# Kernel tuning notes

Hardware: AMD Instinct MI355X
Metric: run time of the kernel (lower is better)

The kernel has to match this reference:

```python
import jax, jax.numpy as jnp
import numpy as np

N, DIM = 65536, 512

def setup_inputs() -> dict:
    key = jax.random.key(0)
    k1, k2, k3 = jax.random.split(key, 3)
    x = jax.random.normal(k1, (N, DIM), dtype=jnp.float32)
    x_fit = jax.random.normal(k2, (N, DIM), dtype=jnp.float32)
    # Module registers S_inv = eye(dim); add a small symmetric PSD perturbation
    # so the matrix is non-trivial while staying well-conditioned.
    A = jax.random.normal(k3, (DIM, DIM), dtype=jnp.float32) / jnp.float32(DIM)
    S_inv = jnp.eye(DIM, dtype=jnp.float32) + A @ A.T
    return {"x": x, "x_fit": x_fit, "S_inv": S_inv}

def reference(x, x_fit, S_inv):
    # Squared Mahalanobis distance per row:
    # diag(delta @ S_inv @ delta.T) == sum((delta @ S_inv) * delta, axis=-1)
    delta = x - x_fit                      # [N, d]
    return jnp.einsum('nd,de,ne->n', delta, S_inv, delta)  # [N]
```

## Files before the change

### kernel.cpp

```cpp
#include <hip/hip_runtime.h>
#include <stdint.h>

#define DIM 512
#define ROWS_PER_BLOCK 64
#define N_CHUNKS 32
#define CHUNK_BYTES 8192
#define WS_BYTES (N_CHUNKS * CHUNK_BYTES)
#define N_BUF 4
#define PREFETCH 3

typedef __attribute__((ext_vector_type(4))) float f32x4;
typedef __attribute__((ext_vector_type(2))) float f32x2;
typedef __attribute__((ext_vector_type(4))) int   i32x4;

static __device__ __forceinline__ int kperm(int kk, int q) {
  int g = q >> 3, j = q & 7;
  int r = (j < 4) ? (g * 4 + j) : (16 + g * 4 + (j - 4));
  return kk * 32 + r;
}

__global__ void prep_R(const float* __restrict__ S, uint32_t* __restrict__ ws) {
  int idx = blockIdx.x * blockDim.x + threadIdx.x;
  if (idx >= WS_BYTES / 4) return;
  int b     = idx * 4;
  int chunk = b >> 13;
  int e_l   = (b >> 9) & 15;
  int inrow = b & 511;
  int slot  = inrow >> 4;
  int bia   = inrow & 15;
  int la    = (slot - e_l) & 31;
  int P = la >> 2, g = la & 3;
  int e = chunk * 16 + e_l;
  float v[4];
#pragma unroll
  for (int t = 0; t < 4; ++t) {
    int bb = bia + t;
    int j  = bb & 7;
    int kk = 2 * P + (bb >> 3);
    int k  = kperm(kk, g * 8 + j);
    v[t] = 64.0f * (S[k * DIM + e] - (k == e ? 1.0f : 0.0f));
  }
  int w = __builtin_amdgcn_cvt_pk_fp8_f32(v[0], v[1], 0, false);
  w     = __builtin_amdgcn_cvt_pk_fp8_f32(v[2], v[3], w, true);
  ws[idx] = (uint32_t)w;
}

static __device__ __forceinline__ void stage_chunk(const uint32_t* __restrict__ ws,
                                                   int eb, char* dst, int tid) {
  const uint32_t* src = ws + (size_t)eb * (CHUNK_BYTES / 4);
#pragma unroll
  for (int r = 0; r < 2; ++r) {
    int idx = r * 256 + tid;
    __builtin_amdgcn_global_load_lds(
        (const __attribute__((address_space(1))) void*)(src + idx * 4),
        (__attribute__((address_space(3))) void*)(dst + idx * 16),
        16, 0, 0);
  }
}

template <int KK>
struct P0 {
  static __device__ __forceinline__ void run(const float* __restrict__ xr,
                                             const float* __restrict__ fr,
                                             int g, long long (&fragL)[16], float& sumsq) {
    const float4 a0 = *(const float4*)(xr + KK * 32 + 4 * g);
    const float4 b0 = *(const float4*)(fr + KK * 32 + 4 * g);
    const float4 a1 = *(const float4*)(xr + KK * 32 + 16 + 4 * g);
    const float4 b1 = *(const float4*)(fr + KK * 32 + 16 + 4 * g);
    float d0 = a0.x - b0.x, d1 = a0.y - b0.y, d2 = a0.z - b0.z, d3 = a0.w - b0.w;
    float d4 = a1.x - b1.x, d5 = a1.y - b1.y, d6 = a1.z - b1.z, d7 = a1.w - b1.w;
    sumsq += d0*d0 + d1*d1 + d2*d2 + d3*d3 + d4*d4 + d5*d5 + d6*d6 + d7*d7;
    int lo = __builtin_amdgcn_cvt_pk_fp8_f32(d0, d1, 0, false);
    lo     = __builtin_amdgcn_cvt_pk_fp8_f32(d2, d3, lo, true);
    int hi = __builtin_amdgcn_cvt_pk_fp8_f32(d4, d5, 0, false);
    hi     = __builtin_amdgcn_cvt_pk_fp8_f32(d6, d7, hi, true);
    fragL[KK] = (long long)(((unsigned long long)(unsigned)hi << 32) | (unsigned)lo);
    P0<KK + 1>::run(xr, fr, g, fragL, sumsq);
  }
};
template <>
struct P0<16> {
  static __device__ __forceinline__ void run(const float*, const float*, int,
                                             long long (&)[16], float&) {}
};

template <int P>
struct KLoop {
  static __device__ __forceinline__ void run(const char* __restrict__ rowbase,
                                             int g, int m,
                                             const long long (&fragL)[16],
                                             f32x4& c0, f32x4& c1) {
    int off = ((4 * P + g + m) & 31) * 16;
    i32x4 a = *(const i32x4*)(rowbase + off);
    long long A0 = (long long)(((unsigned long long)(unsigned)a[1] << 32) | (unsigned)a[0]);
    long long A1 = (long long)(((unsigned long long)(unsigned)a[3] << 32) | (unsigned)a[2]);
    c0 = __builtin_amdgcn_mfma_f32_16x16x32_fp8_fp8(A0, fragL[2 * P],     c0, 0, 0, 0);
    c1 = __builtin_amdgcn_mfma_f32_16x16x32_fp8_fp8(A1, fragL[2 * P + 1], c1, 0, 0, 0);
    KLoop<P + 1>::run(rowbase, g, m, fragL, c0, c1);
  }
};
template <>
struct KLoop<8> {
  static __device__ __forceinline__ void run(const char*, int, int,
                                             const long long (&)[16], f32x4&, f32x4&) {}
};

template <int EB>
struct ChunkLoop {
  static __device__ __forceinline__ void run(const uint32_t* __restrict__ ws,
                                             char* __restrict__ sbase,
                                             int tid, int m, int g,
                                             const long long (&fragL)[16], float& part) {
    if constexpr (EB <= N_CHUNKS - 3)
      asm volatile("s_waitcnt vmcnt(4) lgkmcnt(0)" ::: "memory");
    else if constexpr (EB == N_CHUNKS - 2)
      asm volatile("s_waitcnt vmcnt(2) lgkmcnt(0)" ::: "memory");
    else
      asm volatile("s_waitcnt vmcnt(0) lgkmcnt(0)" ::: "memory");
    __builtin_amdgcn_s_barrier();

    if constexpr (EB + PREFETCH < N_CHUNKS)
      stage_chunk(ws, EB + PREFETCH,
                  sbase + ((EB + PREFETCH) & (N_BUF - 1)) * CHUNK_BYTES, tid);

    const char* rowbase = sbase + (EB & (N_BUF - 1)) * CHUNK_BYTES + m * 512;
    f32x4 c0 = {0.f, 0.f, 0.f, 0.f}, c1 = {0.f, 0.f, 0.f, 0.f};
    KLoop<0>::run(rowbase, g, m, fragL, c0, c1);

    constexpr int kk = EB >> 1;
    int src = (int)(fragL[kk] >> ((EB & 1) * 32));
    f32x2 f01 = __builtin_amdgcn_cvt_pk_f32_fp8(src, false);
    f32x2 f23 = __builtin_amdgcn_cvt_pk_f32_fp8(src, true);
    part += (c0[0] + c1[0]) * f01[0] + (c0[1] + c1[1]) * f01[1]
          + (c0[2] + c1[2]) * f23[0] + (c0[3] + c1[3]) * f23[1];

    ChunkLoop<EB + 1>::run(ws, sbase, tid, m, g, fragL, part);
  }
};
template <>
struct ChunkLoop<N_CHUNKS> {
  static __device__ __forceinline__ void run(const uint32_t*, char*, int, int, int,
                                             const long long (&)[16], float&) {}
};

__global__ __launch_bounds__(256, 2)
void mahal_main(const float* __restrict__ X, const float* __restrict__ XF,
                const uint32_t* __restrict__ ws, float* __restrict__ out) {
  __shared__ __align__(16) char sA[N_BUF][CHUNK_BYTES];

  const int tid  = threadIdx.x;
  const int lane = tid & 63;
  const int wv   = tid >> 6;
  const int m    = lane & 15;
  const int g    = lane >> 4;
  const int row  = blockIdx.x * ROWS_PER_BLOCK + wv * 16 + m;

  const float* xr = X  + (size_t)row * DIM;
  const float* fr = XF + (size_t)row * DIM;

  stage_chunk(ws, 0, sA[0], tid);
  stage_chunk(ws, 1, sA[1], tid);
  stage_chunk(ws, 2, sA[2], tid);

  long long fragL[16];
  float sumsq = 0.f;
  P0<0>::run(xr, fr, g, fragL, sumsq);
  sumsq += __shfl_xor(sumsq, 16);
  sumsq += __shfl_xor(sumsq, 32);

  float part = 0.f;
  ChunkLoop<0>::run(ws, &sA[0][0], tid, m, g, fragL, part);

  part += __shfl_xor(part, 16);
  part += __shfl_xor(part, 32);
  if (g == 0) out[row] = sumsq + part * 0.015625f;
}

__global__ void mahal_naive(const float* __restrict__ X, const float* __restrict__ XF,
                            const float* __restrict__ S, float* __restrict__ out, int n) {
  int row = blockIdx.x * blockDim.x + threadIdx.x;
  if (row >= n) return;
  const float* xr = X + (size_t)row * DIM;
  const float* fr = XF + (size_t)row * DIM;
  float acc = 0.f;
  for (int d = 0; d < DIM; ++d) {
    float dd = xr[d] - fr[d];
    float inner = 0.f;
    for (int e = 0; e < DIM; ++e) inner += S[d * DIM + e] * (xr[e] - fr[e]);
    acc += dd * inner;
  }
  out[row] = acc;
}

extern "C" void kernel_launch(void* const* d_in, const int* in_sizes, int n_in,
                              void* d_out, int out_size, void* d_ws, size_t ws_size,
                              hipStream_t stream) {
  const float* X  = (const float*)d_in[0];
  const float* XF = (const float*)d_in[1];
  const float* S  = (const float*)d_in[2];
  float* out = (float*)d_out;
  const int N = in_sizes[0] / DIM;

  if (ws_size < (size_t)WS_BYTES || (N % ROWS_PER_BLOCK) != 0) {
    mahal_naive<<<(N + 63) / 64, 64, 0, stream>>>(X, XF, S, out, N);
    return;
  }

  uint32_t* ws = (uint32_t*)d_ws;
  prep_R<<<(WS_BYTES / 4 + 255) / 256, 256, 0, stream>>>(S, ws);
  mahal_main<<<N / ROWS_PER_BLOCK, 256, 0, stream>>>(X, XF, ws, out);
}
```

Measured before the change: 304.7 us.

## Split delta computation into coalesced fp8 packing kernel before MFMA pass

Adds a pre-pass kernel that reads x and x_fit with fully coalesced vector loads, computes the delta and its squared norm, and writes a packed fp8 fragment image plus per-row sums into workspace. The main MFMA kernel then loads its fragments from this compact image instead of doing strided fp32 loads and conversions. This removes poorly coalesced fp32 traffic from the latency-sensitive main kernel, at the cost of an extra launch and an extra round trip of the fp8 image through memory. The path is only taken when the workspace is large enough.

Measured after the change: 310.6 us. About the same (+1.9%).

```diff
diff --git a/kernel.cpp b/kernel.cpp
--- a/kernel.cpp
+++ b/kernel.cpp
@@ -43,6 +43,41 @@
   int w = __builtin_amdgcn_cvt_pk_fp8_f32(v[0], v[1], 0, false);
   w     = __builtin_amdgcn_cvt_pk_fp8_f32(v[2], v[3], w, true);
   ws[idx] = (uint32_t)w;
+}
+
+__global__ __launch_bounds__(256)
+void delta_pack(const float* __restrict__ X, const float* __restrict__ XF,
+                unsigned long long* __restrict__ img, float* __restrict__ sums,
+                int nrows) {
+  const int lane = threadIdx.x & 63;
+  const int wid  = blockIdx.x * (blockDim.x >> 6) + (threadIdx.x >> 6);
+  const int nw   = gridDim.x * (blockDim.x >> 6);
+  const int g    = lane & 3;
+  const int h    = (lane >> 2) & 1;
+  const int kA   = lane >> 3;
+  for (int row = wid; row < nrows; row += nw) {
+    const f32x4* xq = (const f32x4*)(X  + (size_t)row * DIM);
+    const f32x4* fq = (const f32x4*)(XF + (size_t)row * DIM);
+    f32x4 xa = xq[lane], fa = fq[lane];
+    f32x4 xb = xq[lane + 64], fb = fq[lane + 64];
+    f32x4 dA = xa - fa, dB = xb - fb;
+    float ps = dA[0]*dA[0] + dA[1]*dA[1] + dA[2]*dA[2] + dA[3]*dA[3]
+             + dB[0]*dB[0] + dB[1]*dB[1] + dB[2]*dB[2] + dB[3]*dB[3];
+    int wA = __builtin_amdgcn_cvt_pk_fp8_f32(dA[0], dA[1], 0, false);
+    wA     = __builtin_amdgcn_cvt_pk_fp8_f32(dA[2], dA[3], wA, true);
+    int wB = __builtin_amdgcn_cvt_pk_fp8_f32(dB[0], dB[1], 0, false);
+    wB     = __builtin_amdgcn_cvt_pk_fp8_f32(dB[2], dB[3], wB, true);
+    int pA = __shfl_xor(wA, 4);
+    int pB = __shfl_xor(wB, 4);
+    unsigned long long L;
+    int kk;
+    if (h == 0) { L = ((unsigned long long)(unsigned)pA << 32) | (unsigned)wA; kk = kA; }
+    else        { L = ((unsigned long long)(unsigned)wB << 32) | (unsigned)pB; kk = 8 + kA; }
+    img[(size_t)row * 64 + g * 16 + kk] = L;
+    ps += __shfl_xor(ps, 1);  ps += __shfl_xor(ps, 2);  ps += __shfl_xor(ps, 4);
+    ps += __shfl_xor(ps, 8);  ps += __shfl_xor(ps, 16); ps += __shfl_xor(ps, 32);
+    if (lane == 0) sums[row] = ps;
+  }
 }
 
 static __device__ __forceinline__ void stage_chunk(const uint32_t* __restrict__ ws,
@@ -143,9 +178,12 @@
                                              const long long (&)[16], float&) {}
 };
 
+template <bool FROM_IMG>
 __global__ __launch_bounds__(256, 2)
 void mahal_main(const float* __restrict__ X, const float* __restrict__ XF,
-                const uint32_t* __restrict__ ws, float* __restrict__ out) {
+                const uint32_t* __restrict__ ws,
+                const unsigned long long* __restrict__ img,
+                const float* __restrict__ sums, float* __restrict__ out) {
   __shared__ __align__(16) char sA[N_BUF][CHUNK_BYTES];
 
   const int tid  = threadIdx.x;
@@ -155,25 +193,39 @@
   const int g    = lane >> 4;
   const int row  = blockIdx.x * ROWS_PER_BLOCK + wv * 16 + m;
 
-  const float* xr = X  + (size_t)row * DIM;
-  const float* fr = XF + (size_t)row * DIM;
-
   stage_chunk(ws, 0, sA[0], tid);
   stage_chunk(ws, 1, sA[1], tid);
   stage_chunk(ws, 2, sA[2], tid);
 
   long long fragL[16];
   float sumsq = 0.f;
-  P0<0>::run(xr, fr, g, fragL, sumsq);
-  sumsq += __shfl_xor(sumsq, 16);
-  sumsq += __shfl_xor(sumsq, 32);
+  if constexpr (FROM_IMG) {
+    const i32x4* ib = (const i32x4*)(img + (size_t)row * 64 + (size_t)g * 16);
+    i32x4 t[8];
+#pragma unroll
+    for (int j = 0; j < 8; ++j) t[j] = ib[j];
+#pragma unroll
+    for (int j = 0; j < 8; ++j) {
+      fragL[2 * j]     = (long long)(((unsigned long long)(unsigned)t[j][1] << 32) | (unsigned)t[j][0]);
+      fragL[2 * j + 1] = (long long)(((unsigned long long)(unsigned)t[j][3] << 32) | (unsigned)t[j][2]);
+    }
+  } else {
+    const float* xr = X  + (size_t)row * DIM;
+    const float* fr = XF + (size_t)row * DIM;
+    P0<0>::run(xr, fr, g, fragL, sumsq);
+    sumsq += __shfl_xor(sumsq, 16);
+    sumsq += __shfl_xor(sumsq, 32);
+  }
 
   float part = 0.f;
   ChunkLoop<0>::run(ws, &sA[0][0], tid, m, g, fragL, part);
 
   part += __shfl_xor(part, 16);
   part += __shfl_xor(part, 32);
-  if (g == 0) out[row] = sumsq + part * 0.015625f;
+  if (g == 0) {
+    float base = FROM_IMG ? sums[row] : sumsq;
+    out[row] = base + part * 0.015625f;
+  }
 }
 
 __global__ void mahal_naive(const float* __restrict__ X, const float* __restrict__ XF,
@@ -201,12 +253,23 @@
   float* out = (float*)d_out;
   const int N = in_sizes[0] / DIM;
 
-  if (ws_size < (size_t)WS_BYTES || (N % ROWS_PER_BLOCK) != 0) {
+  const size_t img_bytes  = (size_t)N * 512;
+  const size_t split_need = (size_t)WS_BYTES + img_bytes + (size_t)N * 4;
+
+  if ((N % ROWS_PER_BLOCK) != 0 || ws_size < (size_t)WS_BYTES) {
     mahal_naive<<<(N + 63) / 64, 64, 0, stream>>>(X, XF, S, out, N);
     return;
   }
 
   uint32_t* ws = (uint32_t*)d_ws;
   prep_R<<<(WS_BYTES / 4 + 255) / 256, 256, 0, stream>>>(S, ws);
-  mahal_main<<<N / ROWS_PER_BLOCK, 256, 0, stream>>>(X, XF, ws, out);
-}
+
+  if (ws_size >= split_need) {
+    unsigned long long* img = (unsigned long long*)((char*)d_ws + WS_BYTES);
+    float* sums = (float*)((char*)d_ws + WS_BYTES + img_bytes);
+    delta_pack<<<2048, 256, 0, stream>>>(X, XF, img, sums, N);
+    mahal_main<true><<<N / ROWS_PER_BLOCK, 256, 0, stream>>>(X, XF, ws, img, sums, out);
+  } else {
+    mahal_main<false><<<N / ROWS_PER_BLOCK, 256, 0, stream>>>(X, XF, ws, nullptr, nullptr, out);
+  }
+}
```
